# Performance work log

Hardware: AMD Instinct MI355X
Metric: run time of the kernel (lower is better)

Reference implementation:

```python
import jax, jax.numpy as jnp
import numpy as np

D = 128      # dim_h
H = 8        # num_heads
DH = D // H  # head dim
G = 32       # graphs in batch
S = 512      # nodes per graph (uniform -> to_dense_batch is a reshape)
N = G * S    # 16384 nodes
DEG = 16
E = N * DEG  # 262144 edges
BN_EPS = 1e-5


def _bn(h, gamma, beta):
    # nn.BatchNorm1d in training mode: per-feature stats over all nodes (biased var)
    mu = jnp.mean(h, axis=0)
    var = jnp.mean((h - mu) ** 2, axis=0)
    return (h - mu) * jax.lax.rsqrt(var + BN_EPS) * gamma + beta


def setup_inputs() -> dict:
    key = jax.random.key(0)
    ks = jax.random.split(key, 10)

    def w(k, shape):  # torch Linear-style uniform(-1/sqrt(fan_in), 1/sqrt(fan_in))
        return jax.random.uniform(k, shape, jnp.float32, -1.0, 1.0) / np.sqrt(shape[-1])

    goff = ((jnp.arange(E) // (E // G)) * S).astype(jnp.int32)  # keep edges within graphs
    src = jax.random.randint(ks[0], (E,), 0, S, jnp.int32) + goff
    dst = jax.random.randint(ks[1], (E,), 0, S, jnp.int32) + goff
    z = lambda n: jnp.zeros((n,), jnp.float32)
    return {
        "x": jax.random.normal(ks[2], (N, D), jnp.float32),
        "edge_index": jnp.stack([src, dst]),
        "edge_attr": jax.random.normal(ks[3], (E, D), jnp.float32),
        "gine_w1": w(ks[4], (D, D)), "gine_b1": z(D),
        "gine_w2": w(ks[5], (D, D)), "gine_b2": z(D),
        "bn1l_gamma": jnp.ones((D,), jnp.float32), "bn1l_beta": z(D),
        "attn_in_w": w(ks[6], (3 * D, D)), "attn_in_b": z(3 * D),
        "attn_out_w": w(ks[7], (D, D)), "attn_out_b": z(D),
        "bn1a_gamma": jnp.ones((D,), jnp.float32), "bn1a_beta": z(D),
        "ff_w1": w(ks[8], (2 * D, D)), "ff_b1": z(2 * D),
        "ff_w2": w(ks[9], (D, 2 * D)), "ff_b2": z(D),
        "bn2_gamma": jnp.ones((D,), jnp.float32), "bn2_beta": z(D),
    }


def reference(x, edge_index, edge_attr,
              gine_w1, gine_b1, gine_w2, gine_b2,
              bn1l_gamma, bn1l_beta,
              attn_in_w, attn_in_b, attn_out_w, attn_out_b,
              bn1a_gamma, bn1a_beta,
              ff_w1, ff_b1, ff_w2, ff_b2,
              bn2_gamma, bn2_beta):
    src, dst = edge_index[0], edge_index[1]

    # --- local branch: GINEConv = mlp((1+eps)*x_i + sum_{j->i} relu(x_j + e_ji)), eps=0
    msg = jax.nn.relu(x[src] + edge_attr)          # [E, D] gather + fused add/relu
    agg = jnp.zeros_like(x).at[dst].add(msg)       # scatter-sum to target nodes
    z = x + agg
    h_gine = jax.nn.relu(z @ gine_w1.T + gine_b1) @ gine_w2.T + gine_b2
    h_local = _bn(x + h_gine, bn1l_gamma, bn1l_beta)   # dropout=0, residual, BN

    # --- global branch: MultiheadAttention over dense per-graph sequences of h_in1
    hd = x.reshape(G, S, D)
    qkv = hd @ attn_in_w.T + attn_in_b             # [G, S, 3D]
    q, k, v = jnp.split(qkv, 3, axis=-1)
    split_heads = lambda t: t.reshape(G, S, H, DH).transpose(0, 2, 1, 3)  # [G,H,S,DH]
    q, k, v = split_heads(q), split_heads(k), split_heads(v)
    att = jax.nn.softmax(jnp.einsum('ghqd,ghkd->ghqk', q, k) / np.sqrt(DH), axis=-1)
    o = jnp.einsum('ghqk,ghkd->ghqd', att, v).transpose(0, 2, 1, 3).reshape(N, D)
    h_attn = _bn(x + (o @ attn_out_w.T + attn_out_b), bn1a_gamma, bn1a_beta)

    # --- combine branches + feed-forward block
    h = h_local + h_attn
    ff = jax.nn.relu(h @ ff_w1.T + ff_b1) @ ff_w2.T + ff_b2
    return _bn(h + ff, bn2_gamma, bn2_beta)
```

## Files before the change

### kernel.cpp

```cpp
#include <hip/hip_runtime.h>
#include <hip/hip_bf16.h>

typedef __attribute__((ext_vector_type(8))) short short8;
typedef __attribute__((ext_vector_type(4))) float f32x4;

#define NN 16384
#define DD 128
#define NE 262144
#define NG 32
#define SS 512
#define NH 8
#define DHD 16
#define EPG 8192
#define BN_EPS 1e-5f

__device__ __forceinline__ unsigned int pk2(float a, float b) {
    union { __hip_bfloat16 h; unsigned short u; } ca, cb;
    ca.h = __float2bfloat16(a);
    cb.h = __float2bfloat16(b);
    return (unsigned int)ca.u | ((unsigned int)cb.u << 16);
}

__global__ __launch_bounds__(512) void build_buckets(
    const int* __restrict__ dst, int* __restrict__ bucket,
    int* __restrict__ start, int* __restrict__ deg)
{
    __shared__ int cnt[512];
    __shared__ int pre[512];
    __shared__ int pre2[512];
    const int g = blockIdx.x;
    const int t = threadIdx.x;
    const int eb = g * EPG;
    cnt[t] = 0;
    __syncthreads();
    #pragma unroll
    for (int i = 0; i < EPG / 512; ++i)
        atomicAdd(&cnt[dst[eb + i * 512 + t] - g * SS], 1);
    __syncthreads();
    int v = cnt[t];
    int* a = pre; int* b = pre2;
    a[t] = v;
    __syncthreads();
    for (int off = 1; off < 512; off <<= 1) {
        int s = a[t] + ((t >= off) ? a[t - off] : 0);
        b[t] = s;
        __syncthreads();
        int* tmp = a; a = b; b = tmp;
    }
    int ex = a[t] - v;
    start[g * SS + t] = ex;
    deg[g * SS + t]   = v;
    cnt[t] = ex;
    __syncthreads();
    #pragma unroll
    for (int i = 0; i < EPG / 512; ++i) {
        int e = eb + i * 512 + t;
        int d = dst[e] - g * SS;
        int p = atomicAdd(&cnt[d], 1);
        bucket[eb + p] = e;
    }
}

__global__ __launch_bounds__(256) void gine_gather(
    const float* __restrict__ x, const int* __restrict__ src,
    const float* __restrict__ ea, const int* __restrict__ bucket,
    const int* __restrict__ start, const int* __restrict__ deg,
    float* __restrict__ z)
{
    const int L = blockIdx.x;
    const int w = (L & 7) * 256 + (L >> 3);
    const int grp = threadIdx.x >> 5;
    const int l   = threadIdx.x & 31;
    const int n   = w * 8 + grp;
    const int g   = n >> 9;
    const int st  = g * EPG + start[n];
    const int de  = deg[n];

    float4 acc = *(const float4*)(x + (size_t)n * DD + l * 4);
    int eid0 = (de > 0) ? bucket[st] : 0;
    int s0   = (de > 0) ? src[eid0] : 0;
    for (int i = 0; i < de; ++i) {
        int eid1 = (i + 1 < de) ? bucket[st + i + 1] : 0;
        int s1   = (i + 1 < de) ? src[eid1] : 0;
        float4 ev = *(const float4*)(ea + (size_t)eid0 * DD + l * 4);
        float4 xv = *(const float4*)(x  + (size_t)s0   * DD + l * 4);
        acc.x += fmaxf(xv.x + ev.x, 0.f);
        acc.y += fmaxf(xv.y + ev.y, 0.f);
        acc.z += fmaxf(xv.z + ev.z, 0.f);
        acc.w += fmaxf(xv.w + ev.w, 0.f);
        eid0 = eid1; s0 = s1;
    }
    *(float4*)(z + (size_t)n * DD + l * 4) = acc;
}

template<bool RELU, bool HAS_RES, bool STATS>
__global__ __launch_bounds__(256) void gemm_bt(
    const float* __restrict__ A,
    const float* __restrict__ W, const float* __restrict__ bias,
    const float* __restrict__ res, float* __restrict__ out,
    float* __restrict__ stats, int K, int Ncols)
{
    constexpr int BK = 64;
    __shared__ unsigned short Ash[128 * BK];
    __shared__ unsigned short Wsh[128 * BK];
    __shared__ float ssh[256];
    const int tid  = threadIdx.x;
    const int lane = tid & 63;
    const int wid  = tid >> 6;
    const int wm   = wid >> 1, wn = wid & 1;
    const int brow = blockIdx.x * 128;
    const int bcol = blockIdx.y * 128;

    f32x4 acc[4][4] = {};

    for (int k0 = 0; k0 < K; k0 += BK) {
        #pragma unroll
        for (int i = 0; i < 4; ++i) {
            int idx = tid + 256 * i;
            int row = idx >> 3;
            int kc  = (idx & 7) * 8;
            int off = row * (BK * 2) + ((kc * 2) ^ ((row & 7) << 4));
            {
                size_t base = (size_t)(brow + row) * K + k0 + kc;
                float4 lo = *(const float4*)(A + base);
                float4 hi = *(const float4*)(A + base + 4);
                int4 pw = { (int)pk2(lo.x, lo.y), (int)pk2(lo.z, lo.w),
                            (int)pk2(hi.x, hi.y), (int)pk2(hi.z, hi.w) };
                *(int4*)((char*)Ash + off) = pw;
            }
            {
                const float* sp = W + (size_t)(bcol + row) * K + k0 + kc;
                float4 lo = *(const float4*)sp;
                float4 hi = *(const float4*)(sp + 4);
                int4 pw = { (int)pk2(lo.x, lo.y), (int)pk2(lo.z, lo.w),
                            (int)pk2(hi.x, hi.y), (int)pk2(hi.z, hi.w) };
                *(int4*)((char*)Wsh + off) = pw;
            }
        }
        __syncthreads();
        #pragma unroll
        for (int ks = 0; ks < BK / 32; ++ks) {
            short8 af[4], bf[4];
            const int kf = ks * 32 + (lane >> 4) * 8;
            #pragma unroll
            for (int mt = 0; mt < 4; ++mt) {
                int row = wm * 64 + mt * 16 + (lane & 15);
                int off = row * (BK * 2) + ((kf * 2) ^ ((row & 7) << 4));
                af[mt] = *(const short8*)((const char*)Ash + off);
            }
            #pragma unroll
            for (int nt = 0; nt < 4; ++nt) {
                int row = wn * 64 + nt * 16 + (lane & 15);
                int off = row * (BK * 2) + ((kf * 2) ^ ((row & 7) << 4));
                bf[nt] = *(const short8*)((const char*)Wsh + off);
            }
            #pragma unroll
            for (int mt = 0; mt < 4; ++mt)
                #pragma unroll
                for (int nt = 0; nt < 4; ++nt)
                    acc[mt][nt] = __builtin_amdgcn_mfma_f32_16x16x32_bf16(
                        af[mt], bf[nt], acc[mt][nt], 0, 0, 0);
        }
        __syncthreads();
    }

    if (STATS) { ssh[tid] = 0.f; __syncthreads(); }

    float cs[4] = {}, cs2[4] = {};
    #pragma unroll
    for (int mt = 0; mt < 4; ++mt) {
        #pragma unroll
        for (int nt = 0; nt < 4; ++nt) {
            int col = bcol + wn * 64 + nt * 16 + (lane & 15);
            float bv = bias[col];
            #pragma unroll
            for (int j = 0; j < 4; ++j) {
                int row = brow + wm * 64 + mt * 16 + (lane >> 4) * 4 + j;
                float v = acc[mt][nt][j] + bv;
                if (RELU) v = fmaxf(v, 0.f);
                if (HAS_RES) v += res[(size_t)row * Ncols + col];
                out[(size_t)row * Ncols + col] = v;
                if (STATS) { cs[nt] += v; cs2[nt] += v * v; }
            }
        }
    }
    if (STATS) {
        #pragma unroll
        for (int nt = 0; nt < 4; ++nt) {
            float s = cs[nt], s2 = cs2[nt];
            s  += __shfl_xor(s, 16);  s  += __shfl_xor(s, 32);
            s2 += __shfl_xor(s2, 16); s2 += __shfl_xor(s2, 32);
            if ((lane >> 4) == 0) {
                int cl = wn * 64 + nt * 16 + (lane & 15);
                atomicAdd(&ssh[cl], s);
                atomicAdd(&ssh[128 + cl], s2);
            }
        }
        __syncthreads();
        if (tid < 128) {
            atomicAdd(&stats[tid], ssh[tid]);
            atomicAdd(&stats[DD + tid], ssh[128 + tid]);
        }
    }
}

__global__ __launch_bounds__(512) void attn_kernel(
    const float* __restrict__ qkv, float* __restrict__ o)
{
    int g = blockIdx.x >> 3;
    int h = blockIdx.x & 7;
    __shared__ float Ksh[SS][DHD];
    __shared__ float Vsh[SS][DHD];
    int t = threadIdx.x;
    const float* rowp = qkv + (size_t)(g * SS + t) * 384;
    {
        const float* kb = rowp + 128 + h * DHD;
        const float* vb = rowp + 256 + h * DHD;
        #pragma unroll
        for (int i = 0; i < 4; ++i) {
            ((float4*)Ksh[t])[i] = ((const float4*)kb)[i];
            ((float4*)Vsh[t])[i] = ((const float4*)vb)[i];
        }
    }
    float q[DHD];
    {
        const float* qb = rowp + h * DHD;
        #pragma unroll
        for (int i = 0; i < 4; ++i) ((float4*)q)[i] = ((const float4*)qb)[i];
    }
    __syncthreads();
    float acc[DHD] = {};
    float l = 0.f;
    for (int j = 0; j < SS; ++j) {
        float s = 0.f;
        #pragma unroll
        for (int d = 0; d < DHD; ++d) s += q[d] * Ksh[j][d];
        float e = __expf(s * 0.25f);
        l += e;
        #pragma unroll
        for (int d = 0; d < DHD; ++d) acc[d] += e * Vsh[j][d];
    }
    float inv = 1.f / l;
    float* ob = o + (size_t)(g * SS + t) * DD + h * DHD;
    #pragma unroll
    for (int d = 0; d < DHD; ++d) acc[d] *= inv;
    #pragma unroll
    for (int i = 0; i < 4; ++i) ((float4*)ob)[i] = ((const float4*)acc)[i];
}

__global__ __launch_bounds__(256) void combine_kernel(
    const float* __restrict__ tl, const float* __restrict__ ta,
    const float* __restrict__ stl, const float* __restrict__ sta,
    const float* __restrict__ g1, const float* __restrict__ b1,
    const float* __restrict__ g2, const float* __restrict__ b2,
    float* __restrict__ out)
{
    int idx = blockIdx.x * 256 + threadIdx.x;
    int c0 = (idx * 4) & (DD - 1);
    float4 vl = ((const float4*)tl)[idx];
    float4 va = ((const float4*)ta)[idx];
    float r[4];
    const float* pl = (const float*)&vl;
    const float* pa = (const float*)&va;
    #pragma unroll
    for (int k = 0; k < 4; ++k) {
        int c = c0 + k;
        float mu1 = stl[c] * (1.f / NN);
        float v1  = stl[DD + c] * (1.f / NN) - mu1 * mu1;
        float rs1 = rsqrtf(v1 + BN_EPS);
        float mu2 = sta[c] * (1.f / NN);
        float v2  = sta[DD + c] * (1.f / NN) - mu2 * mu2;
        float rs2 = rsqrtf(v2 + BN_EPS);
        r[k] = (pl[k] - mu1) * rs1 * g1[c] + b1[c]
             + (pa[k] - mu2) * rs2 * g2[c] + b2[c];
    }
    ((float4*)out)[idx] = *(float4*)r;
}

__global__ __launch_bounds__(256) void final_bn(
    const float* __restrict__ t2, const float* __restrict__ st,
    const float* __restrict__ g, const float* __restrict__ b,
    float* __restrict__ out)
{
    int idx = blockIdx.x * 256 + threadIdx.x;
    int c0 = (idx * 4) & (DD - 1);
    float4 v = ((const float4*)t2)[idx];
    const float* pv = (const float*)&v;
    float r[4];
    #pragma unroll
    for (int k = 0; k < 4; ++k) {
        int c = c0 + k;
        float mu = st[c] * (1.f / NN);
        float va = st[DD + c] * (1.f / NN) - mu * mu;
        float rs = rsqrtf(va + BN_EPS);
        r[k] = (pv[k] - mu) * rs * g[c] + b[c];
    }
    ((float4*)out)[idx] = *(float4*)r;
}

extern "C" void kernel_launch(void* const* d_in, const int* in_sizes, int n_in,
                              void* d_out, int out_size, void* d_ws, size_t ws_size,
                              hipStream_t stream) {
    const float* x    = (const float*)d_in[0];
    const int*   ei   = (const int*)d_in[1];
    const float* ea   = (const float*)d_in[2];
    const float* gw1  = (const float*)d_in[3];
    const float* gb1  = (const float*)d_in[4];
    const float* gw2  = (const float*)d_in[5];
    const float* gb2  = (const float*)d_in[6];
    const float* bn1lg= (const float*)d_in[7];
    const float* bn1lb= (const float*)d_in[8];
    const float* aiw  = (const float*)d_in[9];
    const float* aib  = (const float*)d_in[10];
    const float* aow  = (const float*)d_in[11];
    const float* aob  = (const float*)d_in[12];
    const float* bn1ag= (const float*)d_in[13];
    const float* bn1ab= (const float*)d_in[14];
    const float* fw1  = (const float*)d_in[15];
    const float* fb1  = (const float*)d_in[16];
    const float* fw2  = (const float*)d_in[17];
    const float* fb2  = (const float*)d_in[18];
    const float* bn2g = (const float*)d_in[19];
    const float* bn2b = (const float*)d_in[20];
    float* out = (float*)d_out;
    float* ws  = (float*)d_ws;

    float* regA  = ws;
    float* regB  = ws + 8 * 2097152;
    float* regC  = ws + 10 * 2097152;
    float* regD  = ws + 12 * 2097152;
    float* regE  = ws + 14 * 2097152;
    float* stats = ws + 16 * 2097152;
    float* z     = regA;
    float* qkv   = regA;
    float* f1    = regA;
    int*   bucket= (int*)regB;
    int*   bstart= (int*)regB + NE;
    int*   bdeg  = (int*)regB + NE + NN;
    float* h1    = regB;
    float* o_buf = regB;
    float* t_local = regC;
    float* t2    = regC;
    float* t_attn = regD;
    float* hbuf  = regE;

    hipMemsetAsync(stats, 0, 768 * sizeof(float), stream);

    build_buckets<<<NG, 512, 0, stream>>>(ei + NE, bucket, bstart, bdeg);
    gine_gather<<<NN / 8, 256, 0, stream>>>(x, ei, ea, bucket, bstart, bdeg, z);
    gemm_bt<true, false, false><<<dim3(NN / 128, 1), 256, 0, stream>>>(
        z, gw1, gb1, nullptr, h1, nullptr, 128, 128);
    gemm_bt<false, true, true><<<dim3(NN / 128, 1), 256, 0, stream>>>(
        h1, gw2, gb2, x, t_local, stats, 128, 128);

    gemm_bt<false, false, false><<<dim3(NN / 128, 3), 256, 0, stream>>>(
        x, aiw, aib, nullptr, qkv, nullptr, 128, 384);
    attn_kernel<<<NG * NH, 512, 0, stream>>>(qkv, o_buf);
    gemm_bt<false, true, true><<<dim3(NN / 128, 1), 256, 0, stream>>>(
        o_buf, aow, aob, x, t_attn, stats + 256, 128, 128);

    combine_kernel<<<NN * DD / 4 / 256, 256, 0, stream>>>(
        t_local, t_attn, stats, stats + 256, bn1lg, bn1lb, bn1ag, bn1ab, hbuf);
    gemm_bt<true, false, false><<<dim3(NN / 128, 2), 256, 0, stream>>>(
        hbuf, fw1, fb1, nullptr, f1, nullptr, 128, 256);
    gemm_bt<false, true, true><<<dim3(NN / 128, 1), 256, 0, stream>>>(
        f1, fw2, fb2, hbuf, t2, stats + 512, 256, 128);
    final_bn<<<NN * DD / 4 / 256, 256, 0, stream>>>(t2, stats + 512, bn2g, bn2b, out);
}
```

Measured before the change: 445.8 us.

## Rewrite attention kernel with bf16 MFMA and split query chunks

Replaces the scalar per-thread fp32 attention loop with a wave-level bf16 MFMA kernel: K and transposed V are staged in shared memory as bf16, QK^T and PV are computed with 32x32x16 MFMA, and the probabilities are repacked across lanes with permlane32 swaps. The grid is split into four query chunks per (graph, head), giving more blocks. The aim is to remove the FP32 ALU bound of the scalar dot products. In exchange Q, K, V and P lose precision to bf16, and there is still no max subtraction in the softmax, as before.

```diff
diff --git a/kernel.cpp b/kernel.cpp
--- a/kernel.cpp
+++ b/kernel.cpp
@@ -3,6 +3,7 @@
 
 typedef __attribute__((ext_vector_type(8))) short short8;
 typedef __attribute__((ext_vector_type(4))) float f32x4;
+typedef __attribute__((ext_vector_type(16))) float f32x16;
 
 #define NN 16384
 #define DD 128
@@ -19,6 +20,12 @@
     ca.h = __float2bfloat16(a);
     cb.h = __float2bfloat16(b);
     return (unsigned int)ca.u | ((unsigned int)cb.u << 16);
+}
+
+__device__ __forceinline__ unsigned short bf16u(float f) {
+    union { __hip_bfloat16 h; unsigned short u; } c;
+    c.h = __float2bfloat16(f);
+    return c.u;
 }
 
 __global__ __launch_bounds__(512) void build_buckets(
@@ -204,48 +211,111 @@
     }
 }
 
-__global__ __launch_bounds__(512) void attn_kernel(
+__global__ __launch_bounds__(256) void attn_mfma(
     const float* __restrict__ qkv, float* __restrict__ o)
 {
-    int g = blockIdx.x >> 3;
-    int h = blockIdx.x & 7;
-    __shared__ float Ksh[SS][DHD];
-    __shared__ float Vsh[SS][DHD];
-    int t = threadIdx.x;
-    const float* rowp = qkv + (size_t)(g * SS + t) * 384;
+    __shared__ unsigned short Ksh[SS * 20];
+    __shared__ unsigned short VT[16 * 520];
+    const int id = blockIdx.x;
+    const int g  = ((id >> 3) & 3) * 8 + (id & 7);
+    const int h  = (id >> 5) & 7;
+    const int qc = id >> 8;
+    const int t  = threadIdx.x;
+    const int wid = t >> 6;
+    const int l   = t & 63;
+    const int lq  = l & 31;
+    const int hi  = l >> 5;
+
+    #pragma unroll
+    for (int iter = 0; iter < 2; ++iter) {
+        int key = iter * 256 + t;
+        const float* kp = qkv + (size_t)(g * SS + key) * 384 + 128 + h * DHD;
+        unsigned short us[16];
+        #pragma unroll
+        for (int i = 0; i < 4; ++i) {
+            float4 v = *(const float4*)(kp + i * 4);
+            us[i*4+0] = bf16u(v.x); us[i*4+1] = bf16u(v.y);
+            us[i*4+2] = bf16u(v.z); us[i*4+3] = bf16u(v.w);
+        }
+        unsigned short* kr = Ksh + key * 20;
+        #pragma unroll
+        for (int i = 0; i < 4; ++i) *(uint2*)(kr + i * 4) = *(const uint2*)(us + i * 4);
+        const float* vp = kp + 128;
+        #pragma unroll
+        for (int i = 0; i < 4; ++i) {
+            float4 v = *(const float4*)(vp + i * 4);
+            VT[(i*4+0) * 520 + key] = bf16u(v.x);
+            VT[(i*4+1) * 520 + key] = bf16u(v.y);
+            VT[(i*4+2) * 520 + key] = bf16u(v.z);
+            VT[(i*4+3) * 520 + key] = bf16u(v.w);
+        }
+    }
+
+    const int q0 = qc * 128 + wid * 32;
+    short8 qf;
     {
-        const float* kb = rowp + 128 + h * DHD;
-        const float* vb = rowp + 256 + h * DHD;
-        #pragma unroll
-        for (int i = 0; i < 4; ++i) {
-            ((float4*)Ksh[t])[i] = ((const float4*)kb)[i];
-            ((float4*)Vsh[t])[i] = ((const float4*)vb)[i];
-        }
-    }
-    float q[DHD];
-    {
-        const float* qb = rowp + h * DHD;
-        #pragma unroll
-        for (int i = 0; i < 4; ++i) ((float4*)q)[i] = ((const float4*)qb)[i];
+        const float* qp = qkv + (size_t)(g * SS + q0 + lq) * 384 + h * DHD + hi * 8;
+        float4 a = *(const float4*)qp;
+        float4 b = *(const float4*)(qp + 4);
+        union { unsigned int u[4]; short8 s; } pu;
+        pu.u[0] = pk2(a.x, a.y); pu.u[1] = pk2(a.z, a.w);
+        pu.u[2] = pk2(b.x, b.y); pu.u[3] = pk2(b.z, b.w);
+        qf = pu.s;
     }
     __syncthreads();
-    float acc[DHD] = {};
-    float l = 0.f;
-    for (int j = 0; j < SS; ++j) {
-        float s = 0.f;
-        #pragma unroll
-        for (int d = 0; d < DHD; ++d) s += q[d] * Ksh[j][d];
-        float e = __expf(s * 0.25f);
-        l += e;
-        #pragma unroll
-        for (int d = 0; d < DHD; ++d) acc[d] += e * Vsh[j][d];
-    }
-    float inv = 1.f / l;
-    float* ob = o + (size_t)(g * SS + t) * DD + h * DHD;
-    #pragma unroll
-    for (int d = 0; d < DHD; ++d) acc[d] *= inv;
-    #pragma unroll
-    for (int i = 0; i < 4; ++i) ((float4*)ob)[i] = ((const float4*)acc)[i];
+
+    f32x16 acc = {};
+    const f32x16 zero = {};
+    float lsum = 0.f;
+    for (int kb = 0; kb < 16; ++kb) {
+        short8 kf;
+        {
+            const unsigned short* kr = Ksh + (kb * 32 + lq) * 20 + hi * 8;
+            union { uint2 u[2]; short8 s; } ku;
+            ku.u[0] = *(const uint2*)kr;
+            ku.u[1] = *(const uint2*)(kr + 4);
+            kf = ku.s;
+        }
+        f32x16 st = __builtin_amdgcn_mfma_f32_32x32x16_bf16(kf, qf, zero, 0, 0, 0);
+        float p[16];
+        #pragma unroll
+        for (int j = 0; j < 16; ++j) {
+            p[j] = __expf(st[j] * 0.25f);
+            lsum += p[j];
+        }
+        unsigned int w0 = pk2(p[0],  p[1]),  w1 = pk2(p[2],  p[3]);
+        unsigned int w2 = pk2(p[4],  p[5]),  w3 = pk2(p[6],  p[7]);
+        unsigned int w4 = pk2(p[8],  p[9]),  w5 = pk2(p[10], p[11]);
+        unsigned int w6 = pk2(p[12], p[13]), w7 = pk2(p[14], p[15]);
+        asm("v_permlane32_swap_b32 %0, %1" : "+v"(w0), "+v"(w2));
+        asm("v_permlane32_swap_b32 %0, %1" : "+v"(w1), "+v"(w3));
+        asm("v_permlane32_swap_b32 %0, %1" : "+v"(w4), "+v"(w6));
+        asm("v_permlane32_swap_b32 %0, %1" : "+v"(w5), "+v"(w7));
+        union { unsigned int u[4]; short8 s; } pa0, pa1;
+        pa0.u[0] = w0; pa0.u[1] = w1; pa0.u[2] = w2; pa0.u[3] = w3;
+        pa1.u[0] = w4; pa1.u[1] = w5; pa1.u[2] = w6; pa1.u[3] = w7;
+        const unsigned short* vr = VT + (lq & 15) * 520 + kb * 32 + hi * 8;
+        short8 vf0 = *(const short8*)vr;
+        short8 vf1 = *(const short8*)(vr + 16);
+        acc = __builtin_amdgcn_mfma_f32_32x32x16_bf16(pa0.s, vf0, acc, 0, 0, 0);
+        acc = __builtin_amdgcn_mfma_f32_32x32x16_bf16(pa1.s, vf1, acc, 0, 0, 0);
+    }
+
+    lsum += __shfl_xor(lsum, 32);
+    float rinv = 1.f / lsum;
+    float ov[16];
+    #pragma unroll
+    for (int j = 0; j < 16; ++j) {
+        int row = (j & 3) + 8 * (j >> 2) + 4 * hi;
+        ov[j] = acc[j] * __shfl(rinv, row);
+    }
+    if (lq < DHD) {
+        #pragma unroll
+        for (int j = 0; j < 16; ++j) {
+            int row = (j & 3) + 8 * (j >> 2) + 4 * hi;
+            o[(size_t)(g * SS + q0 + row) * DD + h * DHD + lq] = ov[j];
+        }
+    }
 }
 
 __global__ __launch_bounds__(256) void combine_kernel(
@@ -355,7 +425,7 @@
 
     gemm_bt<false, false, false><<<dim3(NN / 128, 3), 256, 0, stream>>>(
         x, aiw, aib, nullptr, qkv, nullptr, 128, 384);
-    attn_kernel<<<NG * NH, 512, 0, stream>>>(qkv, o_buf);
+    attn_mfma<<<NG * NH * 4, 256, 0, stream>>>(qkv, o_buf);
     gemm_bt<false, true, true><<<dim3(NN / 128, 1), 256, 0, stream>>>(
         o_buf, aow, aob, x, t_attn, stats + 256, 128, 128);
 
```

New measurement: 382.6 us. 1.17x faster.
